# Kernel optimization log

Measured on AMD Instinct MI355X. Metric: run time of the kernel, lower is better.

## Reference

```python
import jax, jax.numpy as jnp
import numpy as np

DIM = 1024
D_STATE = 16

def setup_inputs() -> dict:
    key = jax.random.key(0)
    kx, ka, kd = jax.random.split(key, 3)
    x = jax.random.normal(kx, (4, 8192, DIM), dtype=jnp.float32)
    A = jax.random.normal(ka, (DIM, D_STATE), dtype=jnp.float32)
    D = jax.random.normal(kd, (D_STATE, DIM), dtype=jnp.float32)
    return {"x": x, "A": A, "D": D}

def reference(x, A, D):
    # x: [B, N, C]; A: [C, S]; D: [S, C]
    x_state = jnp.einsum('bnc,cs->bns', x, A)        # [B, N, S]
    x_state = jnp.cumsum(x_state, axis=1)            # prefix sum over sequence
    out = jnp.einsum('bns,sc->bnc', x_state, D)      # [B, N, C]
    return out
```

## Files before the change

### kernel.cpp

```cpp
#include <hip/hip_runtime.h>

#define DIM   1024
#define DST   16
#define NSEQ  8192
#define NB    4

#define K1_MT   64
#define K1_KC   128
#define K1_KCP  132

__global__ __launch_bounds__(256) void k1_gemm(const float* __restrict__ x,
                                               const float* __restrict__ A,
                                               float* __restrict__ T) {
    __shared__ float xs[K1_MT * K1_KCP];
    __shared__ float at[DST * K1_KCP];
    const int t  = threadIdx.x;
    const int b  = blockIdx.x >> 7;
    const int n0 = (blockIdx.x & 127) * K1_MT;
    const int s  = t & 15;
    const int mg = t >> 4;

    const float* xrow = x + ((long)(b * NSEQ + n0)) * DIM;

    float acc0 = 0.f, acc1 = 0.f, acc2 = 0.f, acc3 = 0.f;

    for (int kc = 0; kc < DIM; kc += K1_KC) {
        {
            const int q  = t & 31;
            const int r0 = t >> 5;
            #pragma unroll
            for (int it = 0; it < 8; ++it) {
                const int m = it * 8 + r0;
                const float4 v = *(const float4*)(xrow + (long)m * DIM + kc + 4 * q);
                *(float4*)&xs[m * K1_KCP + 4 * q] = v;
            }
        }
        {
            #pragma unroll
            for (int it = 0; it < 8; ++it) {
                const int idx = it * 256 + t;
                const int kl  = idx >> 4;
                const int ss  = idx & 15;
                at[ss * K1_KCP + kl] = A[(kc + kl) * DST + ss];
            }
        }
        __syncthreads();

        #pragma unroll 4
        for (int kq = 0; kq < K1_KC / 4; ++kq) {
            const float4 a  = *(const float4*)&at[s * K1_KCP + 4 * kq];
            const float4 x0 = *(const float4*)&xs[(mg * 4 + 0) * K1_KCP + 4 * kq];
            const float4 x1 = *(const float4*)&xs[(mg * 4 + 1) * K1_KCP + 4 * kq];
            const float4 x2 = *(const float4*)&xs[(mg * 4 + 2) * K1_KCP + 4 * kq];
            const float4 x3 = *(const float4*)&xs[(mg * 4 + 3) * K1_KCP + 4 * kq];
            acc0 += x0.x * a.x + x0.y * a.y + x0.z * a.z + x0.w * a.w;
            acc1 += x1.x * a.x + x1.y * a.y + x1.z * a.z + x1.w * a.w;
            acc2 += x2.x * a.x + x2.y * a.y + x2.z * a.z + x2.w * a.w;
            acc3 += x3.x * a.x + x3.y * a.y + x3.z * a.z + x3.w * a.w;
        }
        __syncthreads();
    }

    const float4 o = make_float4(acc0, acc1, acc2, acc3);
    *(float4*)&T[((long)(b * DST + s)) * NSEQ + n0 + mg * 4] = o;
}

__global__ __launch_bounds__(256) void k2_scan(float* __restrict__ T) {
    __shared__ float sums[256];
    const int t = threadIdx.x;
    const int b = blockIdx.x >> 4;
    const int s = blockIdx.x & 15;
    float* row = T + ((long)(b * DST + s)) * NSEQ;
    const int base = t * 32;

    float v[32];
    #pragma unroll
    for (int j = 0; j < 8; ++j) {
        const float4 f = *(const float4*)&row[base + 4 * j];
        v[4 * j + 0] = f.x; v[4 * j + 1] = f.y;
        v[4 * j + 2] = f.z; v[4 * j + 3] = f.w;
    }
    float run = 0.f;
    #pragma unroll
    for (int i = 0; i < 32; ++i) { run += v[i]; v[i] = run; }

    sums[t] = run;
    const float total = run;
    __syncthreads();
    for (int off = 1; off < 256; off <<= 1) {
        const float u = (t >= off) ? sums[t - off] : 0.f;
        __syncthreads();
        sums[t] += u;
        __syncthreads();
    }
    const float excl = sums[t] - total;

    #pragma unroll
    for (int j = 0; j < 8; ++j) {
        const float4 f = make_float4(v[4 * j + 0] + excl, v[4 * j + 1] + excl,
                                     v[4 * j + 2] + excl, v[4 * j + 3] + excl);
        *(float4*)&row[base + 4 * j] = f;
    }
}

#define K3_W 64

__global__ __launch_bounds__(256) void k3_out(const float* __restrict__ T,
                                              const float* __restrict__ D,
                                              float* __restrict__ out) {
    __shared__ float sp[K3_W * 20];
    const int t  = threadIdx.x;
    const int b  = blockIdx.x >> 7;
    const int n0 = (blockIdx.x & 127) * K3_W;

    #pragma unroll
    for (int j = 0; j < 4; ++j) {
        const int idx = j * 256 + t;
        const int ss  = idx >> 6;
        const int nn  = idx & 63;
        sp[nn * 20 + ss] = T[((long)(b * DST + ss)) * NSEQ + n0 + nn];
    }

    float4 dreg[16];
    #pragma unroll
    for (int ss = 0; ss < 16; ++ss)
        dreg[ss] = *(const float4*)&D[ss * DIM + 4 * t];

    __syncthreads();

    float* ob = out + ((long)(b * NSEQ + n0)) * DIM + 4 * t;
    for (int r = 0; r < K3_W; ++r) {
        const float4 s0 = *(const float4*)&sp[r * 20 + 0];
        const float4 s1 = *(const float4*)&sp[r * 20 + 4];
        const float4 s2 = *(const float4*)&sp[r * 20 + 8];
        const float4 s3 = *(const float4*)&sp[r * 20 + 12];
        const float sv[16] = {s0.x, s0.y, s0.z, s0.w, s1.x, s1.y, s1.z, s1.w,
                              s2.x, s2.y, s2.z, s2.w, s3.x, s3.y, s3.z, s3.w};
        float4 o = make_float4(0.f, 0.f, 0.f, 0.f);
        #pragma unroll
        for (int ss = 0; ss < 16; ++ss) {
            o.x += sv[ss] * dreg[ss].x;
            o.y += sv[ss] * dreg[ss].y;
            o.z += sv[ss] * dreg[ss].z;
            o.w += sv[ss] * dreg[ss].w;
        }
        *(float4*)(ob + (long)r * DIM) = o;
    }
}

extern "C" void kernel_launch(void* const* d_in, const int* in_sizes, int n_in,
                              void* d_out, int out_size, void* d_ws, size_t ws_size,
                              hipStream_t stream) {
    const float* x = (const float*)d_in[0];
    const float* A = (const float*)d_in[1];
    const float* D = (const float*)d_in[2];
    float* out = (float*)d_out;
    float* T   = (float*)d_ws;

    k1_gemm<<<dim3(NB * 128), dim3(256), 0, stream>>>(x, A, T);
    k2_scan<<<dim3(NB * DST), dim3(256), 0, stream>>>(T);
    k3_out <<<dim3(NB * 128), dim3(256), 0, stream>>>(T, D, out);
}
```

Baseline: 273.4 us.

## Fuse scan into GEMM and output kernels via tile-local scan plus tile-sum prefix

The standalone scan kernel is removed. The GEMM kernel now computes a within-tile prefix sum and writes a per-tile total. The output kernel sums the totals of all preceding tiles to get its base offset and adds it before multiplying by D. This drops one launch and one read-modify-write pass over T, at the cost of redundant prefix summation over tile totals in each output block.

```diff
diff --git a/kernel.cpp b/kernel.cpp
--- a/kernel.cpp
+++ b/kernel.cpp
@@ -5,26 +5,31 @@
 #define NSEQ  8192
 #define NB    4
 
-#define K1_MT   64
-#define K1_KC   128
-#define K1_KCP  132
+#define MT    64
+#define KC    128
+#define KCP   132
+#define NTILE 128
 
-__global__ __launch_bounds__(256) void k1_gemm(const float* __restrict__ x,
-                                               const float* __restrict__ A,
-                                               float* __restrict__ T) {
-    __shared__ float xs[K1_MT * K1_KCP];
-    __shared__ float at[DST * K1_KCP];
-    const int t  = threadIdx.x;
-    const int b  = blockIdx.x >> 7;
-    const int n0 = (blockIdx.x & 127) * K1_MT;
-    const int s  = t & 15;
-    const int mg = t >> 4;
+__global__ __launch_bounds__(256) void kA_gemm_scan(
+    const float* __restrict__ x, const float* __restrict__ A,
+    float* __restrict__ Tloc, float* __restrict__ TS)
+{
+    __shared__ float xs[MT * KCP];
+    __shared__ float at[DST * KCP];
+    __shared__ float scanbuf[16 * DST];
+
+    const int t    = threadIdx.x;
+    const int b    = blockIdx.x >> 7;
+    const int tile = blockIdx.x & 127;
+    const int n0   = tile * MT;
+    const int s    = t & 15;
+    const int mg   = t >> 4;
 
     const float* xrow = x + ((long)(b * NSEQ + n0)) * DIM;
 
     float acc0 = 0.f, acc1 = 0.f, acc2 = 0.f, acc3 = 0.f;
 
-    for (int kc = 0; kc < DIM; kc += K1_KC) {
+    for (int kc = 0; kc < DIM; kc += KC) {
         {
             const int q  = t & 31;
             const int r0 = t >> 5;
@@ -32,7 +37,7 @@
             for (int it = 0; it < 8; ++it) {
                 const int m = it * 8 + r0;
                 const float4 v = *(const float4*)(xrow + (long)m * DIM + kc + 4 * q);
-                *(float4*)&xs[m * K1_KCP + 4 * q] = v;
+                *(float4*)&xs[m * KCP + 4 * q] = v;
             }
         }
         {
@@ -41,18 +46,18 @@
                 const int idx = it * 256 + t;
                 const int kl  = idx >> 4;
                 const int ss  = idx & 15;
-                at[ss * K1_KCP + kl] = A[(kc + kl) * DST + ss];
+                at[ss * KCP + kl] = A[(kc + kl) * DST + ss];
             }
         }
         __syncthreads();
 
         #pragma unroll 4
-        for (int kq = 0; kq < K1_KC / 4; ++kq) {
-            const float4 a  = *(const float4*)&at[s * K1_KCP + 4 * kq];
-            const float4 x0 = *(const float4*)&xs[(mg * 4 + 0) * K1_KCP + 4 * kq];
-            const float4 x1 = *(const float4*)&xs[(mg * 4 + 1) * K1_KCP + 4 * kq];
-            const float4 x2 = *(const float4*)&xs[(mg * 4 + 2) * K1_KCP + 4 * kq];
-            const float4 x3 = *(const float4*)&xs[(mg * 4 + 3) * K1_KCP + 4 * kq];
+        for (int kq = 0; kq < KC / 4; ++kq) {
+            const float4 a  = *(const float4*)&at[s * KCP + 4 * kq];
+            const float4 x0 = *(const float4*)&xs[(mg * 4 + 0) * KCP + 4 * kq];
+            const float4 x1 = *(const float4*)&xs[(mg * 4 + 1) * KCP + 4 * kq];
+            const float4 x2 = *(const float4*)&xs[(mg * 4 + 2) * KCP + 4 * kq];
+            const float4 x3 = *(const float4*)&xs[(mg * 4 + 3) * KCP + 4 * kq];
             acc0 += x0.x * a.x + x0.y * a.y + x0.z * a.z + x0.w * a.w;
             acc1 += x1.x * a.x + x1.y * a.y + x1.z * a.z + x1.w * a.w;
             acc2 += x2.x * a.x + x2.y * a.y + x2.z * a.z + x2.w * a.w;
@@ -61,75 +66,72 @@
         __syncthreads();
     }
 
-    const float4 o = make_float4(acc0, acc1, acc2, acc3);
-    *(float4*)&T[((long)(b * DST + s)) * NSEQ + n0 + mg * 4] = o;
+    const float rsum = acc0 + acc1 + acc2 + acc3;
+    scanbuf[mg * DST + s] = rsum;
+    __syncthreads();
+    float excl = 0.f, total = 0.f;
+    #pragma unroll
+    for (int m = 0; m < 16; ++m) {
+        const float v = scanbuf[m * DST + s];
+        total += v;
+        excl  += (m < mg) ? v : 0.f;
+    }
+    if (mg == 0) TS[((long)b * NTILE + tile) * DST + s] = total;
+
+    const float c0 = excl + acc0;
+    const float c1 = c0 + acc1;
+    const float c2 = c1 + acc2;
+    const float c3 = c2 + acc3;
+    *(float4*)&Tloc[((long)(b * DST + s)) * NSEQ + n0 + mg * 4] =
+        make_float4(c0, c1, c2, c3);
 }
 
-__global__ __launch_bounds__(256) void k2_scan(float* __restrict__ T) {
-    __shared__ float sums[256];
-    const int t = threadIdx.x;
-    const int b = blockIdx.x >> 4;
-    const int s = blockIdx.x & 15;
-    float* row = T + ((long)(b * DST + s)) * NSEQ;
-    const int base = t * 32;
+__global__ __launch_bounds__(256) void kB_scan_out(
+    const float* __restrict__ Tloc, const float* __restrict__ TS,
+    const float* __restrict__ D, float* __restrict__ out)
+{
+    __shared__ float sp[MT * 20];
+    __shared__ float partial[16 * DST];
+    __shared__ float basebuf[DST];
 
-    float v[32];
+    const int t    = threadIdx.x;
+    const int b    = blockIdx.x >> 7;
+    const int tile = blockIdx.x & 127;
+    const int n0   = tile * MT;
+    const int s    = t & 15;
+    const int mg   = t >> 4;
+
+    float4 dreg[16];
     #pragma unroll
-    for (int j = 0; j < 8; ++j) {
-        const float4 f = *(const float4*)&row[base + 4 * j];
-        v[4 * j + 0] = f.x; v[4 * j + 1] = f.y;
-        v[4 * j + 2] = f.z; v[4 * j + 3] = f.w;
+    for (int ss = 0; ss < 16; ++ss)
+        dreg[ss] = *(const float4*)&D[ss * DIM + 4 * t];
+
+    {
+        const float* tsb = TS + (long)b * NTILE * DST;
+        float p = 0.f;
+        for (int j = mg; j < tile; j += 16) p += tsb[j * DST + s];
+        partial[mg * DST + s] = p;
     }
-    float run = 0.f;
-    #pragma unroll
-    for (int i = 0; i < 32; ++i) { run += v[i]; v[i] = run; }
-
-    sums[t] = run;
-    const float total = run;
     __syncthreads();
-    for (int off = 1; off < 256; off <<= 1) {
-        const float u = (t >= off) ? sums[t - off] : 0.f;
-        __syncthreads();
-        sums[t] += u;
-        __syncthreads();
+    {
+        float bsum = 0.f;
+        #pragma unroll
+        for (int m = 0; m < 16; ++m) bsum += partial[m * DST + s];
+        if (mg == 0) basebuf[s] = bsum;
     }
-    const float excl = sums[t] - total;
-
-    #pragma unroll
-    for (int j = 0; j < 8; ++j) {
-        const float4 f = make_float4(v[4 * j + 0] + excl, v[4 * j + 1] + excl,
-                                     v[4 * j + 2] + excl, v[4 * j + 3] + excl);
-        *(float4*)&row[base + 4 * j] = f;
-    }
-}
-
-#define K3_W 64
-
-__global__ __launch_bounds__(256) void k3_out(const float* __restrict__ T,
-                                              const float* __restrict__ D,
-                                              float* __restrict__ out) {
-    __shared__ float sp[K3_W * 20];
-    const int t  = threadIdx.x;
-    const int b  = blockIdx.x >> 7;
-    const int n0 = (blockIdx.x & 127) * K3_W;
+    __syncthreads();
 
     #pragma unroll
     for (int j = 0; j < 4; ++j) {
         const int idx = j * 256 + t;
         const int ss  = idx >> 6;
         const int nn  = idx & 63;
-        sp[nn * 20 + ss] = T[((long)(b * DST + ss)) * NSEQ + n0 + nn];
+        sp[nn * 20 + ss] = Tloc[((long)(b * DST + ss)) * NSEQ + n0 + nn] + basebuf[ss];
     }
-
-    float4 dreg[16];
-    #pragma unroll
-    for (int ss = 0; ss < 16; ++ss)
-        dreg[ss] = *(const float4*)&D[ss * DIM + 4 * t];
-
     __syncthreads();
 
     float* ob = out + ((long)(b * NSEQ + n0)) * DIM + 4 * t;
-    for (int r = 0; r < K3_W; ++r) {
+    for (int r = 0; r < MT; ++r) {
         const float4 s0 = *(const float4*)&sp[r * 20 + 0];
         const float4 s1 = *(const float4*)&sp[r * 20 + 4];
         const float4 s2 = *(const float4*)&sp[r * 20 + 8];
@@ -154,10 +156,10 @@
     const float* x = (const float*)d_in[0];
     const float* A = (const float*)d_in[1];
     const float* D = (const float*)d_in[2];
-    float* out = (float*)d_out;
-    float* T   = (float*)d_ws;
+    float* out  = (float*)d_out;
+    float* Tloc = (float*)d_ws;
+    float* TS   = Tloc + (long)NB * DST * NSEQ;
 
-    k1_gemm<<<dim3(NB * 128), dim3(256), 0, stream>>>(x, A, T);
-    k2_scan<<<dim3(NB * DST), dim3(256), 0, stream>>>(T);
-    k3_out <<<dim3(NB * 128), dim3(256), 0, stream>>>(T, D, out);
+    kA_gemm_scan<<<dim3(NB * NTILE), dim3(256), 0, stream>>>(x, A, Tloc, TS);
+    kB_scan_out <<<dim3(NB * NTILE), dim3(256), 0, stream>>>(Tloc, TS, D, out);
 }
```

Result: no change. 269.6 us (-1.4%).
